# Kernel tuning notes

Hardware: AMD Instinct MI355X
Metric: run time of the kernel (lower is better)

## Reference

```python
import jax, jax.numpy as jnp
import numpy as np

B, A, D = 512, 32, 256      # batch clips, actors (nodes per graph), feature dim
E = 1048576                 # total edges over the flattened (B*A)-node graph
THRESHOLD = 0.5             # config.knn.threshold
EPS = 1e-5


def setup_inputs() -> dict:
    key = jax.random.key(0)
    k1, k2, k3 = jax.random.split(key, 3)
    N = B * A
    X = jax.random.normal(k1, (B, A, D), dtype=jnp.float32)
    edge_index = jax.random.randint(k2, (2, E), 0, N, dtype=jnp.int32)
    W = jax.random.normal(k3, (D, D), dtype=jnp.float32) * (1.0 / np.sqrt(D))
    b = jnp.zeros((D,), dtype=jnp.float32)
    return {"X": X, "edge_index": edge_index, "W": W, "b": b}


def gcn_conv(x, edge_index, W, b):
    # Standard GCNConv: x' = D^-1/2 (A + I) D^-1/2 (x W) + b
    N = x.shape[0]
    x = x @ W                                            # [N, D]
    loop = jnp.arange(N, dtype=edge_index.dtype)
    src = jnp.concatenate([edge_index[0], loop])         # message sources
    tgt = jnp.concatenate([edge_index[1], loop])         # aggregation targets
    deg = jax.ops.segment_sum(jnp.ones_like(src, dtype=x.dtype), tgt,
                              num_segments=N)            # in-degree incl. self-loop
    dinv = jnp.where(deg > 0, jax.lax.rsqrt(deg), 0.0)
    coef = (dinv[src] * dinv[tgt])[:, None]              # symmetric norm per edge
    out = jax.ops.segment_sum(x[src] * coef, tgt, num_segments=N)
    return out + b


def reference(X, edge_index, W, b):
    Bq, Aq, Dq = X.shape
    x = X.reshape(Bq * Aq, Dq)
    x = gcn_conv(x, edge_index, W, b)
    Xo = x.reshape(Bq, Aq, Dq)

    # cal_edge: pairwise squared distances per batch, min-max normalized,
    # thresholded. Instead of variable-length dense_to_sparse edge lists we
    # return the equivalent fixed-shape adjacency mask [B, A, A].
    inner = -2.0 * jnp.einsum('bad,bcd->bac', Xo, Xo)
    sq = jnp.sum(Xo * Xo, axis=-1, keepdims=True)        # [B, A, 1]
    scores = sq + inner + jnp.swapaxes(sq, -1, -2)       # [B, A, A]
    smin = scores.min(axis=-1, keepdims=True)
    smax = scores.max(axis=-1, keepdims=True)
    scores = (scores - smin) / (smax - smin + EPS)
    adj_mask = scores > THRESHOLD                        # new edge set (dense form)
    return Xo, adj_mask
```

## Files before the change

kernel.cpp:

```cpp
#include <hip/hip_runtime.h>

#define BQ 512
#define AQ 32
#define DQ 256
#define NQ (BQ * AQ)
#define EQ 1048576
#define THR 0.5f
#define EPSF 1e-5f
#define DEG_STRIDE 160
#define BIN_TGTS 64
#define NBINS (NQ / BIN_TGTS)
#define BIN_STRIDE 4864

typedef __attribute__((ext_vector_type(8))) short bf16x8;
typedef __attribute__((ext_vector_type(4))) float f32x4;

__device__ __forceinline__ unsigned short f2bf(float f) {
    unsigned int u = __float_as_uint(f);
    return (unsigned short)((u + 0x7FFFu + ((u >> 16) & 1u)) >> 16);
}
__device__ __forceinline__ float bf2f(unsigned short h) {
    return __uint_as_float((unsigned int)h << 16);
}

__global__ __launch_bounds__(256) void k_prep_part(
        const float* __restrict__ W, unsigned short* __restrict__ Wt,
        const int* __restrict__ src, const int* __restrict__ tgt,
        int* __restrict__ bin_cursor, unsigned int* __restrict__ binned) {
    __shared__ int hist[NBINS];
    int tid = threadIdx.x;
    if (blockIdx.x < 256) {
        int idx = blockIdx.x * 256 + tid;
        int n = idx >> 8;
        int k = idx & 255;
        float w = W[k * DQ + n];
        unsigned short h = f2bf(w);
        Wt[idx] = h;
        Wt[DQ * DQ + idx] = f2bf(w - bf2f(h));
        return;
    }
    hist[tid] = 0;
    __syncthreads();
    int base = (blockIdx.x - 256) * 4096;
    int t[16], s[16];
    #pragma unroll
    for (int i = 0; i < 16; i++) {
        int e = base + i * 256 + tid;
        t[i] = tgt[e];
        s[i] = src[e];
        atomicAdd(&hist[t[i] >> 6], 1);
    }
    __syncthreads();
    int mine = hist[tid];
    __syncthreads();
    hist[tid] = tid * BIN_STRIDE + atomicAdd(&bin_cursor[tid], mine);
    __syncthreads();
    #pragma unroll
    for (int i = 0; i < 16; i++) {
        int slot = atomicAdd(&hist[t[i] >> 6], 1);
        binned[slot] = ((unsigned int)t[i] << 14) | (unsigned int)s[i];
    }
}

__global__ __launch_bounds__(256) void k_bucket_gemm(
        const float* __restrict__ Xp, const unsigned short* __restrict__ Wt,
        unsigned short* __restrict__ xwb,
        const int* __restrict__ bin_cursor, const unsigned int* __restrict__ binned,
        unsigned short* __restrict__ bucket, int* __restrict__ cnt,
        float* __restrict__ dinv) {
    __shared__ unsigned short lbuck[BIN_TGTS * DEG_STRIDE];
    __shared__ int lcnt[BIN_TGTS];
    int tid = threadIdx.x;
    if (blockIdx.x < NBINS) {
        int b = blockIdx.x;
        if (tid < BIN_TGTS) lcnt[tid] = 0;
        __syncthreads();
        int beg = b * BIN_STRIDE;
        int count = bin_cursor[b];
        if (count > BIN_STRIDE) count = BIN_STRIDE;
        int end = beg + count;
        for (int i = beg + tid; i < end; i += 256) {
            unsigned int ed = binned[i];
            int tl = (int)(ed >> 14) & 63;
            int pos = atomicAdd(&lcnt[tl], 1);
            if (pos < DEG_STRIDE)
                lbuck[tl * DEG_STRIDE + pos] = (unsigned short)(ed & 0x3FFFu);
        }
        __syncthreads();
        const unsigned int* lb32 = (const unsigned int*)lbuck;
        unsigned int* gb32 = (unsigned int*)(bucket + (size_t)b * BIN_TGTS * DEG_STRIDE);
        #pragma unroll
        for (int i = 0; i < 20; i++) gb32[i * 256 + tid] = lb32[i * 256 + tid];
        if (tid < BIN_TGTS) {
            int c = lcnt[tid];
            cnt[b * BIN_TGTS + tid] = c;
            dinv[b * BIN_TGTS + tid] = rsqrtf((float)(c + 1));
        }
        return;
    }
    int wave = tid >> 6;
    int lane = tid & 63;
    int col = lane & 15;
    int quad = lane >> 4;
    int mbase = (blockIdx.x - NBINS) * 64 + wave * 16;
    int m = mbase + col;

    const float* arow = Xp + (size_t)m * DQ;
    const unsigned short* Wlo = Wt + DQ * DQ;

    f32x4 acc[16];
    f32x4 zero = {0.f, 0.f, 0.f, 0.f};
    #pragma unroll
    for (int i = 0; i < 16; i++) acc[i] = zero;

    for (int k0 = 0; k0 < DQ; k0 += 32) {
        int kq = k0 + quad * 8;
        float4 a0 = *(const float4*)(arow + kq);
        float4 a1 = *(const float4*)(arow + kq + 4);
        float av[8] = {a0.x, a0.y, a0.z, a0.w, a1.x, a1.y, a1.z, a1.w};
        bf16x8 ah, al;
        #pragma unroll
        for (int j = 0; j < 8; j++) {
            unsigned short h = f2bf(av[j]);
            ah[j] = (short)h;
            al[j] = (short)f2bf(av[j] - bf2f(h));
        }
        #pragma unroll
        for (int nt = 0; nt < 16; nt++) {
            size_t boff = (size_t)(nt * 16 + col) * DQ + kq;
            bf16x8 bh = *(const bf16x8*)(Wt + boff);
            bf16x8 bl = *(const bf16x8*)(Wlo + boff);
            acc[nt] = __builtin_amdgcn_mfma_f32_16x16x32_bf16(ah, bh, acc[nt], 0, 0, 0);
            acc[nt] = __builtin_amdgcn_mfma_f32_16x16x32_bf16(al, bh, acc[nt], 0, 0, 0);
            acc[nt] = __builtin_amdgcn_mfma_f32_16x16x32_bf16(ah, bl, acc[nt], 0, 0, 0);
        }
    }

    #pragma unroll
    for (int nt = 0; nt < 16; nt++) {
        #pragma unroll
        for (int r = 0; r < 4; r++) {
            xwb[(size_t)(mbase + quad * 4 + r) * DQ + nt * 16 + col] =
                f2bf(acc[nt][r]);
        }
    }
}

__global__ __launch_bounds__(512) void k_agg_scores(
        const unsigned int* __restrict__ xwb,
        const int* __restrict__ cnt,
        const unsigned short* __restrict__ bucket,
        const float* __restrict__ dinv,
        const float* __restrict__ bias,
        float* __restrict__ out,
        float* __restrict__ mask) {
    __shared__ float xs[AQ][DQ + 4];
    __shared__ float sq[AQ];
    __shared__ float sc[AQ][AQ + 1];
    __shared__ float rmin[AQ], rmax[AQ];

    int tid = threadIdx.x;
    int wave = tid >> 6;
    int lane = tid & 63;
    int bq = blockIdx.x;
    const uint2* xw2 = (const uint2*)xwb;

    float4 bv = ((const float4*)bias)[lane];

    #pragma unroll 1
    for (int i = 0; i < 4; i++) {
        int a = wave * 4 + i;
        int t = bq * AQ + a;
        float dt = dinv[t];
        float c0 = dt * dt;
        uint2 sp = xw2[(size_t)t * 64 + lane];
        float4 acc;
        acc.x = __uint_as_float(sp.x << 16) * c0;
        acc.y = __uint_as_float(sp.x & 0xFFFF0000u) * c0;
        acc.z = __uint_as_float(sp.y << 16) * c0;
        acc.w = __uint_as_float(sp.y & 0xFFFF0000u) * c0;

        const unsigned short* brow = bucket + t * DEG_STRIDE;
        int num = cnt[t];
        if (num > DEG_STRIDE) num = DEG_STRIDE;
        for (int k0 = 0; k0 < num; k0 += 64) {
            int rem = num - k0;
            int n = rem < 64 ? rem : 64;
            int idx = k0 + (lane < n ? lane : 0);
            int e = (int)brow[idx];
            float cl = (lane < n) ? dinv[e] * dt : 0.f;
            int n8 = (n + 7) & ~7;
            for (int j0 = 0; j0 < n8; j0 += 8) {
                #pragma unroll
                for (int jj = 0; jj < 8; jj++) {
                    int j = j0 + jj;
                    int s = __shfl(e, j);
                    float c = __shfl(cl, j);
                    uint2 p = xw2[(size_t)s * 64 + lane];
                    acc.x += __uint_as_float(p.x << 16) * c;
                    acc.y += __uint_as_float(p.x & 0xFFFF0000u) * c;
                    acc.z += __uint_as_float(p.y << 16) * c;
                    acc.w += __uint_as_float(p.y & 0xFFFF0000u) * c;
                }
            }
        }

        acc.x += bv.x; acc.y += bv.y; acc.z += bv.z; acc.w += bv.w;
        ((float4*)out)[(size_t)t * 64 + lane] = acc;
        *(float4*)&xs[a][lane * 4] = acc;
    }
    __syncthreads();

    if (tid < AQ) {
        const float4* xi = (const float4*)xs[tid];
        float s = 0.f;
        #pragma unroll 8
        for (int dd = 0; dd < DQ / 4; dd++) {
            float4 a = xi[dd];
            s += a.x * a.x + a.y * a.y + a.z * a.z + a.w * a.w;
        }
        sq[tid] = s;
    }
    __syncthreads();

    {
        int p0 = tid * 2;
        int i = p0 >> 5;
        int j0 = p0 & 31;
        const float4* xi = (const float4*)xs[i];
        float g[2] = {0.f, 0.f};
        for (int dd = 0; dd < DQ / 4; dd += 8) {
            float4 ar[8];
            #pragma unroll
            for (int u = 0; u < 8; u++) ar[u] = xi[dd + u];
            #pragma unroll
            for (int q = 0; q < 2; q++) {
                const float4* xj = (const float4*)xs[j0 + q];
                float gq = 0.f;
                #pragma unroll
                for (int u = 0; u < 8; u++) {
                    float4 b = xj[dd + u];
                    gq += ar[u].x * b.x + ar[u].y * b.y +
                          ar[u].z * b.z + ar[u].w * b.w;
                }
                g[q] += gq;
            }
        }
        #pragma unroll
        for (int q = 0; q < 2; q++) {
            sc[i][j0 + q] = sq[i] - 2.f * g[q] + sq[j0 + q];
        }
    }
    __syncthreads();

    if (tid < AQ) {
        float mn = sc[tid][0], mx = sc[tid][0];
        for (int j = 1; j < AQ; j++) {
            float v = sc[tid][j];
            mn = fminf(mn, v);
            mx = fmaxf(mx, v);
        }
        rmin[tid] = mn;
        rmax[tid] = mx;
    }
    __syncthreads();

    {
        float* mb = mask + (size_t)bq * AQ * AQ;
        int p0 = tid * 2;
        int i = p0 >> 5, j0 = p0 & 31;
        float inv = 1.0f / (rmax[i] - rmin[i] + EPSF);
        float2 mv;
        mv.x = ((sc[i][j0 + 0] - rmin[i]) * inv > THR) ? 1.0f : 0.0f;
        mv.y = ((sc[i][j0 + 1] - rmin[i]) * inv > THR) ? 1.0f : 0.0f;
        ((float2*)mb)[tid] = mv;
    }
}

extern "C" void kernel_launch(void* const* d_in, const int* in_sizes, int n_in,
                              void* d_out, int out_size, void* d_ws, size_t ws_size,
                              hipStream_t stream) {
    const float* X    = (const float*)d_in[0];
    const int*   ei   = (const int*)d_in[1];
    const float* W    = (const float*)d_in[2];
    const float* bias = (const float*)d_in[3];
    float* out = (float*)d_out;

    char* ws = (char*)d_ws;
    unsigned short* xwb = (unsigned short*)ws;
    unsigned short* bucket = (unsigned short*)(ws + (size_t)NQ * DQ * 2);
    unsigned int* binned = (unsigned int*)(bucket + (size_t)NQ * DEG_STRIDE);
    unsigned short* Wt = (unsigned short*)(binned + (size_t)NBINS * BIN_STRIDE);
    int* cnt = (int*)(Wt + 2 * DQ * DQ);
    float* dinv = (float*)(cnt + NQ);
    int* bin_cursor = (int*)(dinv + NQ);

    const int* src = ei;
    const int* tgt = ei + EQ;

    hipMemsetAsync(bin_cursor, 0, NBINS * sizeof(int), stream);
    k_prep_part<<<512, 256, 0, stream>>>(W, Wt, src, tgt, bin_cursor, binned);
    k_bucket_gemm<<<512, 256, 0, stream>>>(X, Wt, xwb, bin_cursor, binned,
                                           bucket, cnt, dinv);
    k_agg_scores<<<BQ, 512, 0, stream>>>((const unsigned int*)xwb, cnt, bucket,
                                         dinv, bias, out,
                                         out + (size_t)NQ * DQ);
}
```

Before: 187.6 us.

## Replace two-pass binned edge partition with direct global-atomic bucket scatter

Drops the two-pass histogram/bin approach and instead scatters each edge straight into per-target buckets using global atomics on a degree array. The atomic scatter runs alongside the GEMM in one kernel, and dinv is recomputed on the fly from the degree. Deg zeroing moves into the weight-prep kernel, which removes the memset. The aggregation kernel also doubles to 1024 threads with one score pair per thread. This removes a kernel, the binned intermediate and a shared-memory rebucketing pass, at the cost of contended global atomics and scattered 2-byte writes.

```diff
diff --git a/kernel.cpp b/kernel.cpp
--- a/kernel.cpp
+++ b/kernel.cpp
@@ -8,9 +8,6 @@
 #define THR 0.5f
 #define EPSF 1e-5f
 #define DEG_STRIDE 160
-#define BIN_TGTS 64
-#define NBINS (NQ / BIN_TGTS)
-#define BIN_STRIDE 4864
 
 typedef __attribute__((ext_vector_type(8))) short bf16x8;
 typedef __attribute__((ext_vector_type(4))) float f32x4;
@@ -23,78 +20,40 @@
     return __uint_as_float((unsigned int)h << 16);
 }
 
-__global__ __launch_bounds__(256) void k_prep_part(
+__global__ __launch_bounds__(256) void k_wt(
         const float* __restrict__ W, unsigned short* __restrict__ Wt,
+        int* __restrict__ deg) {
+    int tid = threadIdx.x;
+    int idx = blockIdx.x * 256 + tid;
+    int n = idx >> 8;
+    int k = idx & 255;
+    float w = W[k * DQ + n];
+    unsigned short h = f2bf(w);
+    Wt[idx] = h;
+    Wt[DQ * DQ + idx] = f2bf(w - bf2f(h));
+    if (tid < 64) deg[blockIdx.x * 64 + tid] = 0;
+}
+
+__global__ __launch_bounds__(256) void k_scatter_gemm(
+        const float* __restrict__ Xp, const unsigned short* __restrict__ Wt,
+        unsigned short* __restrict__ xwb,
         const int* __restrict__ src, const int* __restrict__ tgt,
-        int* __restrict__ bin_cursor, unsigned int* __restrict__ binned) {
-    __shared__ int hist[NBINS];
+        int* __restrict__ deg, unsigned short* __restrict__ bucket) {
     int tid = threadIdx.x;
     if (blockIdx.x < 256) {
-        int idx = blockIdx.x * 256 + tid;
-        int n = idx >> 8;
-        int k = idx & 255;
-        float w = W[k * DQ + n];
-        unsigned short h = f2bf(w);
-        Wt[idx] = h;
-        Wt[DQ * DQ + idx] = f2bf(w - bf2f(h));
-        return;
-    }
-    hist[tid] = 0;
-    __syncthreads();
-    int base = (blockIdx.x - 256) * 4096;
-    int t[16], s[16];
-    #pragma unroll
-    for (int i = 0; i < 16; i++) {
-        int e = base + i * 256 + tid;
-        t[i] = tgt[e];
-        s[i] = src[e];
-        atomicAdd(&hist[t[i] >> 6], 1);
-    }
-    __syncthreads();
-    int mine = hist[tid];
-    __syncthreads();
-    hist[tid] = tid * BIN_STRIDE + atomicAdd(&bin_cursor[tid], mine);
-    __syncthreads();
-    #pragma unroll
-    for (int i = 0; i < 16; i++) {
-        int slot = atomicAdd(&hist[t[i] >> 6], 1);
-        binned[slot] = ((unsigned int)t[i] << 14) | (unsigned int)s[i];
-    }
-}
-
-__global__ __launch_bounds__(256) void k_bucket_gemm(
-        const float* __restrict__ Xp, const unsigned short* __restrict__ Wt,
-        unsigned short* __restrict__ xwb,
-        const int* __restrict__ bin_cursor, const unsigned int* __restrict__ binned,
-        unsigned short* __restrict__ bucket, int* __restrict__ cnt,
-        float* __restrict__ dinv) {
-    __shared__ unsigned short lbuck[BIN_TGTS * DEG_STRIDE];
-    __shared__ int lcnt[BIN_TGTS];
-    int tid = threadIdx.x;
-    if (blockIdx.x < NBINS) {
-        int b = blockIdx.x;
-        if (tid < BIN_TGTS) lcnt[tid] = 0;
-        __syncthreads();
-        int beg = b * BIN_STRIDE;
-        int count = bin_cursor[b];
-        if (count > BIN_STRIDE) count = BIN_STRIDE;
-        int end = beg + count;
-        for (int i = beg + tid; i < end; i += 256) {
-            unsigned int ed = binned[i];
-            int tl = (int)(ed >> 14) & 63;
-            int pos = atomicAdd(&lcnt[tl], 1);
-            if (pos < DEG_STRIDE)
-                lbuck[tl * DEG_STRIDE + pos] = (unsigned short)(ed & 0x3FFFu);
-        }
-        __syncthreads();
-        const unsigned int* lb32 = (const unsigned int*)lbuck;
-        unsigned int* gb32 = (unsigned int*)(bucket + (size_t)b * BIN_TGTS * DEG_STRIDE);
-        #pragma unroll
-        for (int i = 0; i < 20; i++) gb32[i * 256 + tid] = lb32[i * 256 + tid];
-        if (tid < BIN_TGTS) {
-            int c = lcnt[tid];
-            cnt[b * BIN_TGTS + tid] = c;
-            dinv[b * BIN_TGTS + tid] = rsqrtf((float)(c + 1));
+        int base = blockIdx.x * 4096;
+        int t[16], s[16];
+        #pragma unroll
+        for (int i = 0; i < 16; i++) {
+            int e = base + i * 256 + tid;
+            t[i] = tgt[e];
+            s[i] = src[e];
+        }
+        #pragma unroll
+        for (int i = 0; i < 16; i++) {
+            int slot = atomicAdd(&deg[t[i]], 1);
+            if (slot < DEG_STRIDE)
+                bucket[(size_t)t[i] * DEG_STRIDE + slot] = (unsigned short)s[i];
         }
         return;
     }
@@ -102,7 +61,7 @@
     int lane = tid & 63;
     int col = lane & 15;
     int quad = lane >> 4;
-    int mbase = (blockIdx.x - NBINS) * 64 + wave * 16;
+    int mbase = (blockIdx.x - 256) * 64 + wave * 16;
     int m = mbase + col;
 
     const float* arow = Xp + (size_t)m * DQ;
@@ -146,11 +105,10 @@
     }
 }
 
-__global__ __launch_bounds__(512) void k_agg_scores(
+__global__ __launch_bounds__(1024, 8) void k_agg_scores(
         const unsigned int* __restrict__ xwb,
-        const int* __restrict__ cnt,
+        const int* __restrict__ deg,
         const unsigned short* __restrict__ bucket,
-        const float* __restrict__ dinv,
         const float* __restrict__ bias,
         float* __restrict__ out,
         float* __restrict__ mask) {
@@ -168,10 +126,11 @@
     float4 bv = ((const float4*)bias)[lane];
 
     #pragma unroll 1
-    for (int i = 0; i < 4; i++) {
-        int a = wave * 4 + i;
+    for (int i = 0; i < 2; i++) {
+        int a = wave * 2 + i;
         int t = bq * AQ + a;
-        float dt = dinv[t];
+        int degt = deg[t];
+        float dt = rsqrtf((float)(degt + 1));
         float c0 = dt * dt;
         uint2 sp = xw2[(size_t)t * 64 + lane];
         float4 acc;
@@ -180,15 +139,14 @@
         acc.z = __uint_as_float(sp.y << 16) * c0;
         acc.w = __uint_as_float(sp.y & 0xFFFF0000u) * c0;
 
-        const unsigned short* brow = bucket + t * DEG_STRIDE;
-        int num = cnt[t];
-        if (num > DEG_STRIDE) num = DEG_STRIDE;
+        const unsigned short* brow = bucket + (size_t)t * DEG_STRIDE;
+        int num = degt < DEG_STRIDE ? degt : DEG_STRIDE;
         for (int k0 = 0; k0 < num; k0 += 64) {
             int rem = num - k0;
             int n = rem < 64 ? rem : 64;
             int idx = k0 + (lane < n ? lane : 0);
             int e = (int)brow[idx];
-            float cl = (lane < n) ? dinv[e] * dt : 0.f;
+            float cl = (lane < n) ? rsqrtf((float)(deg[e] + 1)) * dt : 0.f;
             int n8 = (n + 7) & ~7;
             for (int j0 = 0; j0 < n8; j0 += 8) {
                 #pragma unroll
@@ -224,32 +182,22 @@
     __syncthreads();
 
     {
-        int p0 = tid * 2;
-        int i = p0 >> 5;
-        int j0 = p0 & 31;
+        int i = tid >> 5;
+        int j = tid & 31;
         const float4* xi = (const float4*)xs[i];
-        float g[2] = {0.f, 0.f};
+        const float4* xj = (const float4*)xs[j];
+        float g = 0.f;
         for (int dd = 0; dd < DQ / 4; dd += 8) {
-            float4 ar[8];
+            float gq = 0.f;
             #pragma unroll
-            for (int u = 0; u < 8; u++) ar[u] = xi[dd + u];
-            #pragma unroll
-            for (int q = 0; q < 2; q++) {
-                const float4* xj = (const float4*)xs[j0 + q];
-                float gq = 0.f;
-                #pragma unroll
-                for (int u = 0; u < 8; u++) {
-                    float4 b = xj[dd + u];
-                    gq += ar[u].x * b.x + ar[u].y * b.y +
-                          ar[u].z * b.z + ar[u].w * b.w;
-                }
-                g[q] += gq;
+            for (int u = 0; u < 8; u++) {
+                float4 a = xi[dd + u];
+                float4 b = xj[dd + u];
+                gq += a.x * b.x + a.y * b.y + a.z * b.z + a.w * b.w;
             }
-        }
-        #pragma unroll
-        for (int q = 0; q < 2; q++) {
-            sc[i][j0 + q] = sq[i] - 2.f * g[q] + sq[j0 + q];
-        }
+            g += gq;
+        }
+        sc[i][j] = sq[i] - 2.f * g + sq[j];
     }
     __syncthreads();
 
@@ -266,14 +214,11 @@
     __syncthreads();
 
     {
-        float* mb = mask + (size_t)bq * AQ * AQ;
-        int p0 = tid * 2;
-        int i = p0 >> 5, j0 = p0 & 31;
+        int i = tid >> 5;
+        int j = tid & 31;
         float inv = 1.0f / (rmax[i] - rmin[i] + EPSF);
-        float2 mv;
-        mv.x = ((sc[i][j0 + 0] - rmin[i]) * inv > THR) ? 1.0f : 0.0f;
-        mv.y = ((sc[i][j0 + 1] - rmin[i]) * inv > THR) ? 1.0f : 0.0f;
-        ((float2*)mb)[tid] = mv;
+        mask[(size_t)bq * AQ * AQ + tid] =
+            ((sc[i][j] - rmin[i]) * inv > THR) ? 1.0f : 0.0f;
     }
 }
 
@@ -289,20 +234,14 @@
     char* ws = (char*)d_ws;
     unsigned short* xwb = (unsigned short*)ws;
     unsigned short* bucket = (unsigned short*)(ws + (size_t)NQ * DQ * 2);
-    unsigned int* binned = (unsigned int*)(bucket + (size_t)NQ * DEG_STRIDE);
-    unsigned short* Wt = (unsigned short*)(binned + (size_t)NBINS * BIN_STRIDE);
-    int* cnt = (int*)(Wt + 2 * DQ * DQ);
-    float* dinv = (float*)(cnt + NQ);
-    int* bin_cursor = (int*)(dinv + NQ);
+    unsigned short* Wt = bucket + (size_t)NQ * DEG_STRIDE;
+    int* deg = (int*)(Wt + 2 * DQ * DQ);
 
     const int* src = ei;
     const int* tgt = ei + EQ;
 
-    hipMemsetAsync(bin_cursor, 0, NBINS * sizeof(int), stream);
-    k_prep_part<<<512, 256, 0, stream>>>(W, Wt, src, tgt, bin_cursor, binned);
-    k_bucket_gemm<<<512, 256, 0, stream>>>(X, Wt, xwb, bin_cursor, binned,
-                                           bucket, cnt, dinv);
-    k_agg_scores<<<BQ, 512, 0, stream>>>((const unsigned int*)xwb, cnt, bucket,
-                                         dinv, bias, out,
-                                         out + (size_t)NQ * DQ);
-}
+    k_wt<<<256, 256, 0, stream>>>(W, Wt, deg);
+    k_scatter_gemm<<<512, 256, 0, stream>>>(X, Wt, xwb, src, tgt, deg, bucket);
+    k_agg_scores<<<BQ, 1024, 0, stream>>>((const unsigned int*)xwb, deg, bucket,
+                                          bias, out, out + (size_t)NQ * DQ);
+}
```

After: 289.6 us. 1.54x slower.

## Build per-target neighbor lists in aggregation kernel LDS instead of global buckets

Applied to the files above, without the earlier changes.

The second kernel now only counts in-degrees per target to compute dinv, and no longer scatters source indices into a global padded bucket array. The aggregation kernel rebuilds each batch's 32 neighbor lists in shared memory by scanning the 64-target bin that holds that batch and keeping edges whose target falls inside the batch. This drops the global bucket write and read plus the cnt array. In exchange each bin is read twice (by both batch blocks sharing it), and the larger LDS footprint may reduce occupancy of the aggregation kernel.

```diff
diff --git a/kernel.cpp b/kernel.cpp
--- a/kernel.cpp
+++ b/kernel.cpp
@@ -62,40 +62,27 @@
     }
 }
 
-__global__ __launch_bounds__(256) void k_bucket_gemm(
+__global__ __launch_bounds__(256) void k_cnt_gemm(
         const float* __restrict__ Xp, const unsigned short* __restrict__ Wt,
         unsigned short* __restrict__ xwb,
         const int* __restrict__ bin_cursor, const unsigned int* __restrict__ binned,
-        unsigned short* __restrict__ bucket, int* __restrict__ cnt,
         float* __restrict__ dinv) {
-    __shared__ unsigned short lbuck[BIN_TGTS * DEG_STRIDE];
-    __shared__ int lcnt[BIN_TGTS];
     int tid = threadIdx.x;
     if (blockIdx.x < NBINS) {
+        __shared__ int lcnt[BIN_TGTS];
         int b = blockIdx.x;
         if (tid < BIN_TGTS) lcnt[tid] = 0;
         __syncthreads();
         int beg = b * BIN_STRIDE;
         int count = bin_cursor[b];
         if (count > BIN_STRIDE) count = BIN_STRIDE;
-        int end = beg + count;
-        for (int i = beg + tid; i < end; i += 256) {
+        for (int i = beg + tid; i < beg + count; i += 256) {
             unsigned int ed = binned[i];
-            int tl = (int)(ed >> 14) & 63;
-            int pos = atomicAdd(&lcnt[tl], 1);
-            if (pos < DEG_STRIDE)
-                lbuck[tl * DEG_STRIDE + pos] = (unsigned short)(ed & 0x3FFFu);
+            atomicAdd(&lcnt[(ed >> 14) & 63], 1);
         }
         __syncthreads();
-        const unsigned int* lb32 = (const unsigned int*)lbuck;
-        unsigned int* gb32 = (unsigned int*)(bucket + (size_t)b * BIN_TGTS * DEG_STRIDE);
-        #pragma unroll
-        for (int i = 0; i < 20; i++) gb32[i * 256 + tid] = lb32[i * 256 + tid];
-        if (tid < BIN_TGTS) {
-            int c = lcnt[tid];
-            cnt[b * BIN_TGTS + tid] = c;
-            dinv[b * BIN_TGTS + tid] = rsqrtf((float)(c + 1));
-        }
+        if (tid < BIN_TGTS)
+            dinv[b * BIN_TGTS + tid] = rsqrtf((float)(lcnt[tid] + 1));
         return;
     }
     int wave = tid >> 6;
@@ -148,8 +135,8 @@
 
 __global__ __launch_bounds__(512) void k_agg_scores(
         const unsigned int* __restrict__ xwb,
-        const int* __restrict__ cnt,
-        const unsigned short* __restrict__ bucket,
+        const unsigned int* __restrict__ binned,
+        const int* __restrict__ bin_cursor,
         const float* __restrict__ dinv,
         const float* __restrict__ bias,
         float* __restrict__ out,
@@ -158,12 +145,33 @@
     __shared__ float sq[AQ];
     __shared__ float sc[AQ][AQ + 1];
     __shared__ float rmin[AQ], rmax[AQ];
+    __shared__ unsigned short lbuck[AQ * DEG_STRIDE];
+    __shared__ int lcnt[AQ];
 
     int tid = threadIdx.x;
     int wave = tid >> 6;
     int lane = tid & 63;
     int bq = blockIdx.x;
     const uint2* xw2 = (const uint2*)xwb;
+
+    if (tid < AQ) lcnt[tid] = 0;
+    __syncthreads();
+    {
+        int b = bq >> 1;
+        int beg = b * BIN_STRIDE;
+        int count = bin_cursor[b];
+        if (count > BIN_STRIDE) count = BIN_STRIDE;
+        for (int i = beg + tid; i < beg + count; i += 512) {
+            unsigned int ed = binned[i];
+            if ((int)(ed >> 19) == bq) {
+                int a = (ed >> 14) & 31;
+                int pos = atomicAdd(&lcnt[a], 1);
+                if (pos < DEG_STRIDE)
+                    lbuck[a * DEG_STRIDE + pos] = (unsigned short)(ed & 0x3FFFu);
+            }
+        }
+    }
+    __syncthreads();
 
     float4 bv = ((const float4*)bias)[lane];
 
@@ -180,14 +188,13 @@
         acc.z = __uint_as_float(sp.y << 16) * c0;
         acc.w = __uint_as_float(sp.y & 0xFFFF0000u) * c0;
 
-        const unsigned short* brow = bucket + t * DEG_STRIDE;
-        int num = cnt[t];
+        int num = lcnt[a];
         if (num > DEG_STRIDE) num = DEG_STRIDE;
         for (int k0 = 0; k0 < num; k0 += 64) {
             int rem = num - k0;
             int n = rem < 64 ? rem : 64;
             int idx = k0 + (lane < n ? lane : 0);
-            int e = (int)brow[idx];
+            int e = (int)lbuck[a * DEG_STRIDE + idx];
             float cl = (lane < n) ? dinv[e] * dt : 0.f;
             int n8 = (n + 7) & ~7;
             for (int j0 = 0; j0 < n8; j0 += 8) {
@@ -288,11 +295,9 @@
 
     char* ws = (char*)d_ws;
     unsigned short* xwb = (unsigned short*)ws;
-    unsigned short* bucket = (unsigned short*)(ws + (size_t)NQ * DQ * 2);
-    unsigned int* binned = (unsigned int*)(bucket + (size_t)NQ * DEG_STRIDE);
+    unsigned int* binned = (unsigned int*)(ws + (size_t)NQ * DQ * 2);
     unsigned short* Wt = (unsigned short*)(binned + (size_t)NBINS * BIN_STRIDE);
-    int* cnt = (int*)(Wt + 2 * DQ * DQ);
-    float* dinv = (float*)(cnt + NQ);
+    float* dinv = (float*)(Wt + 2 * DQ * DQ);
     int* bin_cursor = (int*)(dinv + NQ);
 
     const int* src = ei;
@@ -300,9 +305,8 @@
 
     hipMemsetAsync(bin_cursor, 0, NBINS * sizeof(int), stream);
     k_prep_part<<<512, 256, 0, stream>>>(W, Wt, src, tgt, bin_cursor, binned);
-    k_bucket_gemm<<<512, 256, 0, stream>>>(X, Wt, xwb, bin_cursor, binned,
-                                           bucket, cnt, dinv);
-    k_agg_scores<<<BQ, 512, 0, stream>>>((const unsigned int*)xwb, cnt, bucket,
-                                         dinv, bias, out,
+    k_cnt_gemm<<<512, 256, 0, stream>>>(X, Wt, xwb, bin_cursor, binned, dinv);
+    k_agg_scores<<<BQ, 512, 0, stream>>>((const unsigned int*)xwb, binned,
+                                         bin_cursor, dinv, bias, out,
                                          out + (size_t)NQ * DQ);
 }
```

Result: no change. 189.0 us (+0.7%).
